# Kernel optimization log

Hardware: AMD Instinct MI355X
Metric: run time of the kernel (lower is better)

## Reference

```python
import jax, jax.numpy as jnp
import numpy as np

H = 2; C = 64          # heads, hidden_channels
N = 50000; E = 800000  # nodes, edges
D = 128                # input_dim
EPS = 1e-5

def _lrelu(x, s):
    return jnp.where(x >= 0, x, s * x)

def _ln(x, g, b):
    m = x.mean(-1, keepdims=True)
    v = ((x - m) ** 2).mean(-1, keepdims=True)
    return (x - m) / jnp.sqrt(v + EPS) * g + b

def _gatv2(x_src, x_dst, src, dst, Wl, bl, Wr, br, att, Wres, bias):
    # PyG GATv2Conv: concat=False (mean over heads), residual=True, no self loops
    n = x_dst.shape[0]
    xl = (x_src @ Wl + bl).reshape(-1, H, C)  # [Ns,H,C]
    xr = (x_dst @ Wr + br).reshape(-1, H, C)  # [Nd,H,C]
    xj = xl[src]                               # [E,H,C] messages from source
    xi = xr[dst]                               # [E,H,C]
    e = _lrelu(xi + xj, 0.2)
    alpha = jnp.einsum('ehc,hc->eh', e, att)   # [E,H]
    amax = jax.lax.stop_gradient(jax.ops.segment_max(alpha, dst, num_segments=n))
    ex = jnp.exp(alpha - amax[dst])
    den = jax.ops.segment_sum(ex, dst, num_segments=n)
    a = ex / den[dst]                          # segment softmax over incoming edges
    out = jax.ops.segment_sum(xj * a[:, :, None], dst, num_segments=n)  # [Nd,H,C]
    return out.mean(axis=1) + x_dst @ Wres + bias


def setup_inputs() -> dict:
    key = jax.random.key(0)
    ks = jax.random.split(key, 40)
    d = {}
    d['x'] = jax.random.normal(ks[0], (N, D), jnp.float32)
    d['edge_index'] = jax.random.randint(ks[1], (2, E), 0, N, jnp.int32)
    i = 2
    for p, ind in (('c1d', D), ('c1t', D), ('c2d', C), ('c2t', C)):
        d[p + '_Wl'] = jax.random.normal(ks[i], (ind, H * C), jnp.float32) * 0.05; i += 1
        d[p + '_bl'] = jnp.zeros((H * C,), jnp.float32)
        d[p + '_Wr'] = jax.random.normal(ks[i], (ind, H * C), jnp.float32) * 0.05; i += 1
        d[p + '_br'] = jnp.zeros((H * C,), jnp.float32)
        d[p + '_att'] = jax.random.normal(ks[i], (H, C), jnp.float32) * 0.05; i += 1
        d[p + '_Wres'] = jax.random.normal(ks[i], (ind, C), jnp.float32) * 0.05; i += 1
        d[p + '_bias'] = jnp.zeros((C,), jnp.float32)
    d['nd_g'] = jnp.ones((C,), jnp.float32); d['nd_b'] = jnp.zeros((C,), jnp.float32)
    d['nt_g'] = jnp.ones((C,), jnp.float32); d['nt_b'] = jnp.zeros((C,), jnp.float32)
    return d


def reference(x, edge_index, c1d_Wl, c1d_bl, c1d_Wr, c1d_br, c1d_att, c1d_Wres, c1d_bias, c1t_Wl, c1t_bl, c1t_Wr, c1t_br, c1t_att, c1t_Wres, c1t_bias, c2d_Wl, c2d_bl, c2d_Wr, c2d_br, c2d_att, c2d_Wres, c2d_bias, c2t_Wl, c2t_bl, c2t_Wr, c2t_br, c2t_att, c2t_Wres, c2t_bias, nd_g, nd_b, nt_g, nt_b):
    src, dst = edge_index[0], edge_index[1]
    dep = _gatv2(x, x, src, dst, c1d_Wl, c1d_bl, c1d_Wr, c1d_br, c1d_att, c1d_Wres, c1d_bias)
    dep = _lrelu(_ln(dep, nd_g, nd_b), 0.01)
    dant = _gatv2(x, x, dst, src, c1t_Wl, c1t_bl, c1t_Wr, c1t_br, c1t_att, c1t_Wres, c1t_bias)
    dant = _lrelu(_ln(dant, nt_g, nt_b), 0.01)
    dep2 = _lrelu(_gatv2(dep, dep, src, dst, c2d_Wl, c2d_bl, c2d_Wr, c2d_br, c2d_att, c2d_Wres, c2d_bias), 0.01)
    dant2 = _lrelu(_gatv2(dant, dant, dst, src, c2t_Wl, c2t_bl, c2t_Wr, c2t_br, c2t_att, c2t_Wres, c2t_bias), 0.01)
    return jnp.concatenate([dep2, dant2, x], axis=-1)
```

## Files before the change

### kernel.cpp

```cpp
#include <hip/hip_runtime.h>
#include <math.h>

typedef unsigned short ushort_t;
typedef unsigned char uchar_t;
typedef __attribute__((ext_vector_type(8))) short short8x;
typedef __attribute__((ext_vector_type(4))) float f32x4;
typedef __attribute__((ext_vector_type(2))) float f32x2;

#define CSHIFT 9
#define CC 12288
#define EPB 4096
#define ECAP 1024
#define NCMAX 128

__device__ __forceinline__ unsigned f2bf(float f) {
  unsigned u = __float_as_uint(f);
  u += 0x7fff + ((u >> 16) & 1);
  return u >> 16;
}
__device__ __forceinline__ float bf2f(ushort_t u) {
  return __uint_as_float(((unsigned)u) << 16);
}
__device__ __forceinline__ float dpp_red8(float v) {
  v += __int_as_float(__builtin_amdgcn_update_dpp(0, __float_as_int(v), 0xB1, 0xF, 0xF, true));
  v += __int_as_float(__builtin_amdgcn_update_dpp(0, __float_as_int(v), 0x4E, 0xF, 0xF, true));
  v += __int_as_float(__builtin_amdgcn_update_dpp(0, __float_as_int(v), 0x141, 0xF, 0xF, true));
  return v;
}

struct GArgs {
  const float* Wl[2];
  const float* bl[2];
  const float* Wr[2];
  const float* br[2];
  const float* Wres[2];
  const float* bias[2];
};

__device__ __forceinline__ float wval1(const GArgs& ga, int col, int k) {
  int dir = col >= 320 ? 1 : 0;
  int cc = col - dir * 320;
  return cc < 128 ? ga.Wl[dir][k * 128 + cc]
       : cc < 256 ? ga.Wr[dir][k * 128 + (cc - 128)]
                  : ga.Wres[dir][k * 64 + (cc - 256)];
}
__device__ __forceinline__ float bval(const GArgs& ga, int col) {
  int dir = col >= 320 ? 1 : 0;
  int cc = col - dir * 320;
  return cc < 128 ? ga.bl[dir][cc]
       : cc < 256 ? ga.br[dir][cc - 128]
                  : ga.bias[dir][cc - 256];
}


__global__ __launch_bounds__(128) void pack_kernel(GArgs g1, GArgs g2,
                                                   ushort_t* __restrict__ WT1,
                                                   ushort_t* __restrict__ WT2,
                                                   float* __restrict__ bc1,
                                                   float* __restrict__ bc2) {
  int b = blockIdx.x;
  int k = threadIdx.x;
  if (b < 640) {
    WT1[b * 128 + k] = (ushort_t)f2bf(wval1(g1, b, k));
  } else if (b < 1280) {
    int c = b - 640;
    int dir = c >= 320 ? 1 : 0;
    int cc = c - dir * 320;
    float v = 0.f;
    if ((k >> 6) == dir) {
      int k2 = k & 63;
      v = cc < 128 ? g2.Wl[dir][k2 * 128 + cc]
        : cc < 256 ? g2.Wr[dir][k2 * 128 + (cc - 128)]
                   : g2.Wres[dir][k2 * 64 + (cc - 256)];
    }
    WT2[c * 128 + k] = (ushort_t)f2bf(v);
  } else {
    for (int c = k; c < 640; c += 128) {
      bc1[c] = bval(g1, c);
      bc2[c] = bval(g2, c);
    }
  }
}


template <int AF32>
__device__ __forceinline__ void gemm_body(const float* Af, const ushort_t* Ab,
                                          const ushort_t* WT, const float* bc,
                                          ushort_t* Y, uchar_t* XL8, int N,
                                          int rb, int cb, ushort_t* lds) {
  const int tid = threadIdx.x;
  const int lane = tid & 63;
  const int w = tid >> 6;
  const int m0 = rb * 64;
  const int cbase = cb * 128 + w * 32;

#pragma unroll
  for (int c = 0; c < 4; ++c) {
    int Lb = (tid + c * 256) * 16;
    int row = Lb >> 8, within = Lb & 255;
    int so = within ^ ((row & 7) << 4);
    int grow = m0 + row;
    if (grow >= N) grow = N - 1;
    if (AF32) {
      const float* src = Af + (size_t)grow * 128 + (so >> 1);
      float4 a = *(const float4*)src;
      float4 b = *(const float4*)(src + 4);
      uint4 o;
      o.x = f2bf(a.x) | (f2bf(a.y) << 16);
      o.y = f2bf(a.z) | (f2bf(a.w) << 16);
      o.z = f2bf(b.x) | (f2bf(b.y) << 16);
      o.w = f2bf(b.z) | (f2bf(b.w) << 16);
      ((uint4*)lds)[tid + c * 256] = o;
    } else {
      ((uint4*)lds)[tid + c * 256] = *(const uint4*)(Ab + (size_t)grow * 128 + (so >> 1));
    }
  }

  short8x bf[4][2];
#pragma unroll
  for (int ks = 0; ks < 4; ++ks)
#pragma unroll
    for (int ns = 0; ns < 2; ++ns) {
      int col = cbase + ns * 16 + (lane & 15);
      bf[ks][ns] = *(const short8x*)(WT + (size_t)col * 128 + ks * 32 + (lane >> 4) * 8);
    }

  __syncthreads();

  f32x4 z = {0.f, 0.f, 0.f, 0.f};
  f32x4 acc[4][2];
#pragma unroll
  for (int ms = 0; ms < 4; ++ms) {
    acc[ms][0] = z;
    acc[ms][1] = z;
  }
#pragma unroll
  for (int ks = 0; ks < 4; ++ks) {
    short8x af[4];
#pragma unroll
    for (int ms = 0; ms < 4; ++ms) {
      int row = ms * 16 + (lane & 15);
      int byte = row * 256 + ((ks * 64 + (lane >> 4) * 16) ^ ((row & 7) << 4));
      af[ms] = *(const short8x*)((const char*)lds + byte);
    }
#pragma unroll
    for (int ms = 0; ms < 4; ++ms) {
      acc[ms][0] = __builtin_amdgcn_mfma_f32_16x16x32_bf16(af[ms], bf[ks][0], acc[ms][0], 0, 0, 0);
      acc[ms][1] = __builtin_amdgcn_mfma_f32_16x16x32_bf16(af[ms], bf[ks][1], acc[ms][1], 0, 0, 0);
    }
  }

#pragma unroll
  for (int ms = 0; ms < 4; ++ms)
#pragma unroll
    for (int ns = 0; ns < 2; ++ns) {
      int col = cbase + ns * 16 + (lane & 15);
      float bv = bc[col];
      int dir = col >= 320 ? 1 : 0;
      int cc = col - dir * 320;
#pragma unroll
      for (int r = 0; r < 4; ++r) {
        int grow = m0 + ms * 16 + (lane >> 4) * 4 + r;
        if (grow < N) {
          float val = acc[ms][ns][r] + bv;
          if (cc < 128) {
            int pk = __builtin_amdgcn_cvt_pk_fp8_f32(val, val, 0, false);
            XL8[(size_t)grow * 256 + dir * 128 + cc] = (uchar_t)(pk & 0xff);
          } else {
            Y[(size_t)grow * 640 + col] = (ushort_t)f2bf(val);
          }
        }
      }
    }
}


__global__ __launch_bounds__(256) void k_front(
    const float* __restrict__ x, const int* __restrict__ ei, int E, int N,
    int* __restrict__ gc0, int* __restrict__ gc1, int* __restrict__ ctail0,
    int* __restrict__ ctail1, const ushort_t* __restrict__ WT1,
    const float* __restrict__ bc1, ushort_t* __restrict__ Y,
    uchar_t* __restrict__ XL8, float* __restrict__ out, int nbinA, int ngemm,
    int nrow) {
  __shared__ ushort_t lds[8192];
  const int bid = blockIdx.x;
  const int t = threadIdx.x;
  if (bid < nbinA) {
    int* h0 = (int*)lds;
    int* h1 = h0 + NCMAX;
    int* b0 = h1 + NCMAX;
    int* b1 = b0 + NCMAX;
    const int e0 = bid * EPB;
    const int e1 = min(e0 + EPB, E);
    for (int i = t; i < NCMAX; i += 256) {
      h0[i] = 0;
      h1[i] = 0;
    }
    __syncthreads();
    for (int i = e0 + t; i < e1; i += 256) {
      int s = ei[i], d = ei[E + i];
      atomicAdd(&h0[d >> CSHIFT], 1);
      atomicAdd(&h1[s >> CSHIFT], 1);
    }
    __syncthreads();
    for (int c = t; c < NCMAX; c += 256) {
      int n0 = h0[c], n1 = h1[c];
      b0[c] = n0 ? atomicAdd(&ctail0[c], n0) : 0;
      b1[c] = n1 ? atomicAdd(&ctail1[c], n1) : 0;
      h0[c] = 0;
      h1[c] = 0;
    }
    __syncthreads();
    for (int i = e0 + t; i < e1; i += 256) {
      int s = ei[i], d = ei[E + i];
      int c0 = d >> CSHIFT;
      int p0 = b0[c0] + atomicAdd(&h0[c0], 1);
      if (p0 < CC) gc0[c0 * CC + p0] = (s << 16) | d;
      int c1 = s >> CSHIFT;
      int p1 = b1[c1] + atomicAdd(&h1[c1], 1);
      if (p1 < CC) gc1[c1 * CC + p1] = (d << 16) | s;
    }
  } else if (bid < nbinA + ngemm) {
    int gb = bid - nbinA;
    gemm_body<1>(x, nullptr, WT1, bc1, Y, XL8, N, gb % nrow, gb / nrow, lds);
  } else {
    int i = (bid - nbinA - ngemm) * 256 + t;
    if (i < N * 32) {
      float4 v = ((const float4*)x)[i];
      ((float4*)out)[(size_t)(i >> 5) * 64 + 32 + (i & 31)] = v;
    }
  }
}


__global__ __launch_bounds__(256) void gemm2_kernel(const ushort_t* __restrict__ A,
                                                    const ushort_t* __restrict__ WT,
                                                    const float* __restrict__ bc,
                                                    ushort_t* __restrict__ Y,
                                                    uchar_t* __restrict__ XL8, int N) {
  __shared__ ushort_t lds[8192];
  gemm_body<0>(nullptr, A, WT, bc, Y, XL8, N, blockIdx.x, blockIdx.y, lds);
}


template <int MODE>
__global__ __launch_bounds__(256) void agg_bucket(
    const ushort_t* __restrict__ Y, const uchar_t* __restrict__ XL8,
    const int* __restrict__ gc0, const int* __restrict__ gc1,
    const int* __restrict__ ctail0, const int* __restrict__ ctail1,
    const float* __restrict__ attA, const float* __restrict__ attB,
    const float* __restrict__ lng0, const float* __restrict__ lnb0,
    const float* __restrict__ lng1, const float* __restrict__ lnb1,
    void* __restrict__ outp, int N) {
  __shared__ int ebuf[ECAP];
  __shared__ int lnbr[ECAP + 8];
  __shared__ int hist[32], offs[32], cur[32];
  __shared__ int ecnt;
  const int fb = blockIdx.x;
  const int cb = fb >> 4;
  const int dir = blockIdx.y;
  const int t = threadIdx.x;
  const int* gc = dir ? gc1 : gc0;
  const int* ctail = dir ? ctail1 : ctail0;
  const float* att = dir ? attB : attA;

  for (int i = t; i < ECAP + 8; i += 256) lnbr[i] = 0;
  if (t < 32) {
    hist[t] = 0;
    cur[t] = 0;
  }
  if (t == 64) ecnt = 0;
  __syncthreads();

  {
    const int cntc = min(ctail[cb], CC);
    const int* src = gc + cb * CC;
    const int iters = (cntc + 255) >> 8;
    for (int it = 0; it < iters; ++it) {
      int i = it * 256 + t;
      int e = 0;
      bool m = false;
      if (i < cntc) {
        e = src[i];
        m = ((e & 0xFFFF) >> 5) == fb;
      }
      unsigned long long mk = __ballot(m);
      int cnt = __popcll(mk);
      int base = 0;
      if ((t & 63) == 0 && cnt) base = atomicAdd(&ecnt, cnt);
      base = __shfl(base, 0);
      if (m) {
        int pos = base + __popcll(mk & ((1ull << (t & 63)) - 1));
        if (pos < ECAP) ebuf[pos] = e;
      }
    }
  }
  __syncthreads();
  const int tot = min(ecnt, ECAP);
  for (int i = t; i < tot; i += 256) atomicAdd(&hist[ebuf[i] & 31], 1);
  __syncthreads();
  if (t < 32) {
    int v = hist[t], inc = v;
#pragma unroll
    for (int o = 1; o < 32; o <<= 1) {
      int u = __shfl_up(inc, o);
      if (t >= o) inc += u;
    }
    offs[t] = inc - v;
  }
  __syncthreads();
  for (int i = t; i < tot; i += 256) {
    int e = ebuf[i];
    int r = e & 31;
    lnbr[offs[r] + atomicAdd(&cur[r], 1)] = (int)((unsigned)e >> 16) * 256;
  }
  __syncthreads();

  const int wv = t >> 6, lane = t & 63, g = lane >> 4, jj = lane & 15;
  const float L2E = 1.4426950408889634f;
  float av[8];
  {
    float4 a0 = *(const float4*)(att + jj * 8);
    float4 a1 = *(const float4*)(att + jj * 8 + 4);
    av[0] = a0.x * L2E; av[1] = a0.y * L2E; av[2] = a0.z * L2E; av[3] = a0.w * L2E;
    av[4] = a1.x * L2E; av[5] = a1.y * L2E; av[6] = a1.z * L2E; av[7] = a1.w * L2E;
  }
  const uchar_t* X8b = XL8 + dir * 128 + jj * 8;

  for (int r = wv; r < 32; r += 4) {
    const int n = fb * 32 + r;
    if (n >= N) break;
    const char* rowp = (const char*)Y + (size_t)n * 1280 + dir * 640;

    float xi[8];
    {
      short8x v = *(const short8x*)(rowp + 256 + jj * 16);
#pragma unroll
      for (int q = 0; q < 8; ++q) xi[q] = bf2f((ushort_t)v[q]);
    }
    float d = 0.f;
    float acc[8];
#pragma unroll
    for (int q = 0; q < 8; ++q) acc[q] = 0.f;

    const int beg = offs[r], deg = hist[r];
    if (deg > 0) {
      int off = lnbr[beg + g];
      uint2 v8 = *(const uint2*)(X8b + (size_t)(unsigned)off);
      for (int k0 = 0; k0 < deg; k0 += 4) {
        int offn = lnbr[beg + k0 + 4 + g];
        uint2 vn = *(const uint2*)(X8b + (size_t)(unsigned)offn);
        f32x2 x01 = __builtin_amdgcn_cvt_pk_f32_fp8((int)v8.x, false);
        f32x2 x23 = __builtin_amdgcn_cvt_pk_f32_fp8((int)v8.x, true);
        f32x2 x45 = __builtin_amdgcn_cvt_pk_f32_fp8((int)v8.y, false);
        f32x2 x67 = __builtin_amdgcn_cvt_pk_f32_fp8((int)v8.y, true);
        float xj[8] = {x01[0], x01[1], x23[0], x23[1],
                       x45[0], x45[1], x67[0], x67[1]};
        float p = 0.f;
#pragma unroll
        for (int q = 0; q < 8; ++q) {
          float e = xi[q] + xj[q];
          e = fmaxf(e, 0.2f * e);
          p = fmaf(e, av[q], p);
        }
        p = dpp_red8(p);
        float wgt = (k0 + g < deg) ? __builtin_amdgcn_exp2f(p) : 0.f;
        d += wgt;
#pragma unroll
        for (int q = 0; q < 8; ++q) acc[q] = fmaf(xj[q], wgt, acc[q]);
        v8 = vn;
      }
#pragma unroll
      for (int o = 16; o <= 32; o <<= 1) {
        d += __shfl_xor(d, o);
#pragma unroll
        for (int q = 0; q < 8; ++q) acc[q] += __shfl_xor(acc[q], o);
      }
    }
    float inv = deg > 0 ? 1.f / d : 0.f;
    float v[8];
#pragma unroll
    for (int q = 0; q < 8; ++q) {
      float tq = acc[q] * inv;
      v[q] = 0.5f * (tq + __shfl_xor(tq, 8));
    }
    {
      short8x rv = *(const short8x*)(rowp + 512 + (jj & 7) * 16);
#pragma unroll
      for (int q = 0; q < 8; ++q) v[q] += bf2f((ushort_t)rv[q]);
    }

    if (MODE == 0) {
      float s = 0.f;
#pragma unroll
      for (int q = 0; q < 8; ++q) s += v[q];
      s += __shfl_xor(s, 1);
      s += __shfl_xor(s, 2);
      s += __shfl_xor(s, 4);
      float mu = s * (1.f / 64.f);
      float vs = 0.f;
#pragma unroll
      for (int q = 0; q < 8; ++q) {
        float dv = v[q] - mu;
        vs += dv * dv;
      }
      vs += __shfl_xor(vs, 1);
      vs += __shfl_xor(vs, 2);
      vs += __shfl_xor(vs, 4);
      float rstd = rsqrtf(vs * (1.f / 64.f) + 1e-5f);
      if (g == 0 && jj < 8) {
        const float* lg = dir ? lng1 : lng0;
        const float* lb = dir ? lnb1 : lnb0;
        unsigned o2[8];
#pragma unroll
        for (int q = 0; q < 8; ++q) {
          int c = jj * 8 + q;
          float y = (v[q] - mu) * rstd * lg[c] + lb[c];
          y = fmaxf(y, 0.01f * y);
          o2[q] = f2bf(y);
        }
        uint4 pk;
        pk.x = o2[0] | (o2[1] << 16);
        pk.y = o2[2] | (o2[3] << 16);
        pk.z = o2[4] | (o2[5] << 16);
        pk.w = o2[6] | (o2[7] << 16);
        *(uint4*)((ushort_t*)outp + (size_t)n * 128 + dir * 64 + jj * 8) = pk;
      }
    } else {
      if (g == 0 && jj < 8) {
        float* op = (float*)outp + (size_t)n * 256 + dir * 64 + jj * 8;
        float4 o0, o1;
        o0.x = fmaxf(v[0], 0.01f * v[0]);
        o0.y = fmaxf(v[1], 0.01f * v[1]);
        o0.z = fmaxf(v[2], 0.01f * v[2]);
        o0.w = fmaxf(v[3], 0.01f * v[3]);
        o1.x = fmaxf(v[4], 0.01f * v[4]);
        o1.y = fmaxf(v[5], 0.01f * v[5]);
        o1.z = fmaxf(v[6], 0.01f * v[6]);
        o1.w = fmaxf(v[7], 0.01f * v[7]);
        *(float4*)op = o0;
        *(float4*)(op + 4) = o1;
      }
    }
  }
}


extern "C" void kernel_launch(void* const* d_in, const int* in_sizes, int n_in,
                              void* d_out, int out_size, void* d_ws, size_t ws_size,
                              hipStream_t stream) {
  const float* x = (const float*)d_in[0];
  const int* ei = (const int*)d_in[1];
  const int N = in_sizes[0] / 128;
  const int E = in_sizes[1] / 2;
  float* out = (float*)d_out;
  const int nbuck = (N + 31) >> 5;
  const int ncoarse = (N + (1 << CSHIFT) - 1) >> CSHIFT;

  char* p = (char*)d_ws;
  auto carve = [&](size_t bytes) {
    char* q = p;
    p += ((bytes + 255) & ~(size_t)255);
    return q;
  };
  int* ctail = (int*)carve(2 * NCMAX * 4);
  int* gc0 = (int*)carve((size_t)ncoarse * CC * 4);
  int* gc1 = (int*)carve((size_t)ncoarse * CC * 4);
  ushort_t* Y1 = (ushort_t*)carve((size_t)N * 640 * 2);
  uchar_t* XL8 = (uchar_t*)carve((size_t)N * 256);
  ushort_t* A2 = (ushort_t*)carve((size_t)N * 128 * 2);
  ushort_t* WT1 = (ushort_t*)carve(640 * 128 * 2);
  ushort_t* WT2 = (ushort_t*)carve(640 * 128 * 2);
  float* bc1 = (float*)carve(640 * 4);
  float* bc2 = (float*)carve(640 * 4);
  int* ctail0 = ctail;
  int* ctail1 = ctail + NCMAX;

  auto F = [&](int i) { return (const float*)d_in[i]; };
  GArgs g1, g2;
  g1.Wl[0] = F(2);  g1.bl[0] = F(3);  g1.Wr[0] = F(4);  g1.br[0] = F(5);
  g1.Wres[0] = F(7); g1.bias[0] = F(8);
  g1.Wl[1] = F(9);  g1.bl[1] = F(10); g1.Wr[1] = F(11); g1.br[1] = F(12);
  g1.Wres[1] = F(14); g1.bias[1] = F(15);
  g2.Wl[0] = F(16); g2.bl[0] = F(17); g2.Wr[0] = F(18); g2.br[0] = F(19);
  g2.Wres[0] = F(21); g2.bias[0] = F(22);
  g2.Wl[1] = F(23); g2.bl[1] = F(24); g2.Wr[1] = F(25); g2.br[1] = F(26);
  g2.Wres[1] = F(28); g2.bias[1] = F(29);

  hipMemsetAsync(ctail, 0, 2 * NCMAX * 4, stream);

  pack_kernel<<<1281, 128, 0, stream>>>(g1, g2, WT1, WT2, bc1, bc2);

  const int nbinA = (E + EPB - 1) / EPB;
  const int nrow = (N + 63) / 64;
  const int ngemm = nrow * 5;
  const int ncopy = (N * 32 + 255) / 256;
  k_front<<<nbinA + ngemm + ncopy, 256, 0, stream>>>(
      x, ei, E, N, gc0, gc1, ctail0, ctail1, WT1, bc1, Y1, XL8, out,
      nbinA, ngemm, nrow);

  const dim3 ga(nbuck, 2);
  agg_bucket<0><<<ga, 256, 0, stream>>>(Y1, XL8, gc0, gc1, ctail0, ctail1,
                                        F(6), F(13), F(30), F(31), F(32), F(33),
                                        A2, N);
  gemm2_kernel<<<dim3(nrow, 5), 256, 0, stream>>>(A2, WT2, bc2, Y1, XL8, N);
  agg_bucket<1><<<ga, 256, 0, stream>>>(Y1, XL8, gc0, gc1, ctail0, ctail1,
                                        F(20), F(27), nullptr, nullptr, nullptr,
                                        nullptr, out, N);
}
```

Before: 309.8 us.

## Use 64-node fine buckets, XCD-aware block mapping, and deeper gather prefetch

```diff
diff --git a/kernel.cpp b/kernel.cpp
--- a/kernel.cpp
+++ b/kernel.cpp
@@ -10,7 +10,7 @@
 #define CSHIFT 9
 #define CC 12288
 #define EPB 4096
-#define ECAP 1024
+#define ECAP 2048
 #define NCMAX 128
 
 __device__ __forceinline__ unsigned f2bf(float f) {
@@ -251,21 +251,27 @@
     const float* __restrict__ attA, const float* __restrict__ attB,
     const float* __restrict__ lng0, const float* __restrict__ lnb0,
     const float* __restrict__ lng1, const float* __restrict__ lnb1,
-    void* __restrict__ outp, int N) {
+    void* __restrict__ outp, int ncoarse, int N) {
   __shared__ int ebuf[ECAP];
-  __shared__ int lnbr[ECAP + 8];
-  __shared__ int hist[32], offs[32], cur[32];
+  __shared__ int lnbr[ECAP + 24];
+  __shared__ int hist[64], offs[64], cur[64];
   __shared__ int ecnt;
-  const int fb = blockIdx.x;
-  const int cb = fb >> 4;
+  const int bid = blockIdx.x;
+  const int xcd = bid & 7;
+  const int q = bid >> 3;
+  const int cb = (q >> 3) * 8 + xcd;
+  const int fi = q & 7;
+  if (cb >= ncoarse) return;
+  const int fb = cb * 8 + fi;
+  if (fb * 64 >= N) return;
   const int dir = blockIdx.y;
   const int t = threadIdx.x;
   const int* gc = dir ? gc1 : gc0;
   const int* ctail = dir ? ctail1 : ctail0;
   const float* att = dir ? attB : attA;
 
-  for (int i = t; i < ECAP + 8; i += 256) lnbr[i] = 0;
-  if (t < 32) {
+  for (int i = t; i < ECAP + 24; i += 256) lnbr[i] = 0;
+  if (t < 64) {
     hist[t] = 0;
     cur[t] = 0;
   }
@@ -282,7 +288,7 @@
       bool m = false;
       if (i < cntc) {
         e = src[i];
-        m = ((e & 0xFFFF) >> 5) == fb;
+        m = ((e & 0xFFFF) >> 6) == fb;
       }
       unsigned long long mk = __ballot(m);
       int cnt = __popcll(mk);
@@ -297,12 +303,12 @@
   }
   __syncthreads();
   const int tot = min(ecnt, ECAP);
-  for (int i = t; i < tot; i += 256) atomicAdd(&hist[ebuf[i] & 31], 1);
+  for (int i = t; i < tot; i += 256) atomicAdd(&hist[ebuf[i] & 63], 1);
   __syncthreads();
-  if (t < 32) {
+  if (t < 64) {
     int v = hist[t], inc = v;
 #pragma unroll
-    for (int o = 1; o < 32; o <<= 1) {
+    for (int o = 1; o < 64; o <<= 1) {
       int u = __shfl_up(inc, o);
       if (t >= o) inc += u;
     }
@@ -311,7 +317,7 @@
   __syncthreads();
   for (int i = t; i < tot; i += 256) {
     int e = ebuf[i];
-    int r = e & 31;
+    int r = e & 63;
     lnbr[offs[r] + atomicAdd(&cur[r], 1)] = (int)((unsigned)e >> 16) * 256;
   }
   __syncthreads();
@@ -327,8 +333,8 @@
   }
   const uchar_t* X8b = XL8 + dir * 128 + jj * 8;
 
-  for (int r = wv; r < 32; r += 4) {
-    const int n = fb * 32 + r;
+  for (int r = wv; r < 64; r += 4) {
+    const int n = fb * 64 + r;
     if (n >= N) break;
     const char* rowp = (const char*)Y + (size_t)n * 1280 + dir * 640;
 
@@ -336,72 +342,75 @@
     {
       short8x v = *(const short8x*)(rowp + 256 + jj * 16);
 #pragma unroll
-      for (int q = 0; q < 8; ++q) xi[q] = bf2f((ushort_t)v[q]);
+      for (int q2 = 0; q2 < 8; ++q2) xi[q2] = bf2f((ushort_t)v[q2]);
     }
     float d = 0.f;
     float acc[8];
 #pragma unroll
-    for (int q = 0; q < 8; ++q) acc[q] = 0.f;
+    for (int q2 = 0; q2 < 8; ++q2) acc[q2] = 0.f;
 
     const int beg = offs[r], deg = hist[r];
     if (deg > 0) {
-      int off = lnbr[beg + g];
-      uint2 v8 = *(const uint2*)(X8b + (size_t)(unsigned)off);
+      int oA = lnbr[beg + g];
+      int oB = lnbr[beg + 4 + g];
+      uint2 vC = *(const uint2*)(X8b + (size_t)(unsigned)oA);
+      uint2 vD = *(const uint2*)(X8b + (size_t)(unsigned)oB);
       for (int k0 = 0; k0 < deg; k0 += 4) {
-        int offn = lnbr[beg + k0 + 4 + g];
-        uint2 vn = *(const uint2*)(X8b + (size_t)(unsigned)offn);
-        f32x2 x01 = __builtin_amdgcn_cvt_pk_f32_fp8((int)v8.x, false);
-        f32x2 x23 = __builtin_amdgcn_cvt_pk_f32_fp8((int)v8.x, true);
-        f32x2 x45 = __builtin_amdgcn_cvt_pk_f32_fp8((int)v8.y, false);
-        f32x2 x67 = __builtin_amdgcn_cvt_pk_f32_fp8((int)v8.y, true);
+        int oN = lnbr[beg + k0 + 8 + g];
+        uint2 vN = *(const uint2*)(X8b + (size_t)(unsigned)oN);
+        f32x2 x01 = __builtin_amdgcn_cvt_pk_f32_fp8((int)vC.x, false);
+        f32x2 x23 = __builtin_amdgcn_cvt_pk_f32_fp8((int)vC.x, true);
+        f32x2 x45 = __builtin_amdgcn_cvt_pk_f32_fp8((int)vC.y, false);
+        f32x2 x67 = __builtin_amdgcn_cvt_pk_f32_fp8((int)vC.y, true);
         float xj[8] = {x01[0], x01[1], x23[0], x23[1],
                        x45[0], x45[1], x67[0], x67[1]};
         float p = 0.f;
 #pragma unroll
-        for (int q = 0; q < 8; ++q) {
-          float e = xi[q] + xj[q];
+        for (int q2 = 0; q2 < 8; ++q2) {
+          float e = xi[q2] + xj[q2];
           e = fmaxf(e, 0.2f * e);
-          p = fmaf(e, av[q], p);
+          p = fmaf(e, av[q2], p);
         }
         p = dpp_red8(p);
         float wgt = (k0 + g < deg) ? __builtin_amdgcn_exp2f(p) : 0.f;
         d += wgt;
 #pragma unroll
-        for (int q = 0; q < 8; ++q) acc[q] = fmaf(xj[q], wgt, acc[q]);
-        v8 = vn;
+        for (int q2 = 0; q2 < 8; ++q2) acc[q2] = fmaf(xj[q2], wgt, acc[q2]);
+        vC = vD;
+        vD = vN;
       }
 #pragma unroll
       for (int o = 16; o <= 32; o <<= 1) {
         d += __shfl_xor(d, o);
 #pragma unroll
-        for (int q = 0; q < 8; ++q) acc[q] += __shfl_xor(acc[q], o);
+        for (int q2 = 0; q2 < 8; ++q2) acc[q2] += __shfl_xor(acc[q2], o);
       }
     }
     float inv = deg > 0 ? 1.f / d : 0.f;
     float v[8];
 #pragma unroll
-    for (int q = 0; q < 8; ++q) {
-      float tq = acc[q] * inv;
-      v[q] = 0.5f * (tq + __shfl_xor(tq, 8));
+    for (int q2 = 0; q2 < 8; ++q2) {
+      float tq = acc[q2] * inv;
+      v[q2] = 0.5f * (tq + __shfl_xor(tq, 8));
     }
     {
       short8x rv = *(const short8x*)(rowp + 512 + (jj & 7) * 16);
 #pragma unroll
-      for (int q = 0; q < 8; ++q) v[q] += bf2f((ushort_t)rv[q]);
+      for (int q2 = 0; q2 < 8; ++q2) v[q2] += bf2f((ushort_t)rv[q2]);
     }
 
     if (MODE == 0) {
       float s = 0.f;
 #pragma unroll
-      for (int q = 0; q < 8; ++q) s += v[q];
+      for (int q2 = 0; q2 < 8; ++q2) s += v[q2];
       s += __shfl_xor(s, 1);
       s += __shfl_xor(s, 2);
       s += __shfl_xor(s, 4);
       float mu = s * (1.f / 64.f);
       float vs = 0.f;
 #pragma unroll
-      for (int q = 0; q < 8; ++q) {
-        float dv = v[q] - mu;
+      for (int q2 = 0; q2 < 8; ++q2) {
+        float dv = v[q2] - mu;
         vs += dv * dv;
       }
       vs += __shfl_xor(vs, 1);
@@ -413,11 +422,11 @@
         const float* lb = dir ? lnb1 : lnb0;
         unsigned o2[8];
 #pragma unroll
-        for (int q = 0; q < 8; ++q) {
-          int c = jj * 8 + q;
-          float y = (v[q] - mu) * rstd * lg[c] + lb[c];
+        for (int q2 = 0; q2 < 8; ++q2) {
+          int c = jj * 8 + q2;
+          float y = (v[q2] - mu) * rstd * lg[c] + lb[c];
           y = fmaxf(y, 0.01f * y);
-          o2[q] = f2bf(y);
+          o2[q2] = f2bf(y);
         }
         uint4 pk;
         pk.x = o2[0] | (o2[1] << 16);
@@ -454,7 +463,6 @@
   const int N = in_sizes[0] / 128;
   const int E = in_sizes[1] / 2;
   float* out = (float*)d_out;
-  const int nbuck = (N + 31) >> 5;
   const int ncoarse = (N + (1 << CSHIFT) - 1) >> CSHIFT;
 
   char* p = (char*)d_ws;
@@ -499,12 +507,13 @@
       x, ei, E, N, gc0, gc1, ctail0, ctail1, WT1, bc1, Y1, XL8, out,
       nbinA, ngemm, nrow);
 
-  const dim3 ga(nbuck, 2);
+  const int pcb8 = ((ncoarse + 7) / 8) * 8;
+  const dim3 ga(pcb8 * 8, 2);
   agg_bucket<0><<<ga, 256, 0, stream>>>(Y1, XL8, gc0, gc1, ctail0, ctail1,
                                         F(6), F(13), F(30), F(31), F(32), F(33),
-                                        A2, N);
+                                        A2, ncoarse, N);
   gemm2_kernel<<<dim3(nrow, 5), 256, 0, stream>>>(A2, WT2, bc2, Y1, XL8, N);
   agg_bucket<1><<<ga, 256, 0, stream>>>(Y1, XL8, gc0, gc1, ctail0, ctail1,
                                         F(20), F(27), nullptr, nullptr, nullptr,
-                                        nullptr, out, N);
-}
+                                        nullptr, out, ncoarse, N);
+}
```

After: 303.9 us, median of 2. Within noise of the previous version (-1.9%).
